# Kernel optimization log

Hardware: AMD Instinct MI355X
Metric: run time of the kernel (lower is better)

Reference implementation:

```python
import jax, jax.numpy as jnp
import numpy as np

N_USER = 100000
N_RECIPE = 50000
E = 1000000
H = 128


def setup_inputs() -> dict:
    key = jax.random.key(0)
    ks = jax.random.split(key, 5)
    z_user = jax.random.normal(ks[0], (N_USER, H), dtype=jnp.float32)
    z_recipe = jax.random.normal(ks[1], (N_RECIPE, H), dtype=jnp.float32)
    edge_label_index = jax.random.randint(ks[2], (2, E), 0, N_RECIPE, dtype=jnp.int64)
    W1 = jax.random.normal(ks[3], (2 * H, H), dtype=jnp.float32) * (1.0 / np.sqrt(2 * H))
    b1 = jnp.zeros((H,), dtype=jnp.float32)
    W2 = jax.random.normal(ks[4], (H, 1), dtype=jnp.float32) * (1.0 / np.sqrt(H))
    b2 = jnp.zeros((1,), dtype=jnp.float32)
    return {"z_user": z_user, "z_recipe": z_recipe,
            "edge_label_index": edge_label_index,
            "W1": W1, "b1": b1, "W2": W2, "b2": b2}


def reference(z_user, z_recipe, edge_label_index, W1, b1, W2, b2):
    row, col = edge_label_index[0], edge_label_index[1]
    # gather + concat: [E, 2H]
    z = jnp.concatenate([z_user[row], z_recipe[col]], axis=-1)
    h = jax.nn.relu(z @ W1 + b1)        # [E, H]
    out = h @ W2 + b2                    # [E, 1]
    return out.reshape(-1)
```

## Files before the change

kernel.cpp:

```cpp
#include <hip/hip_runtime.h>
#include <hip/hip_bf16.h>


#define HDIM 128

typedef __attribute__((ext_vector_type(8))) __bf16 bf16x8;
typedef __attribute__((ext_vector_type(16))) float f32x16;

static __device__ __forceinline__ unsigned short bf16_bits(float x) {
  return __builtin_bit_cast(unsigned short, static_cast<__bf16>(x));
}

static __device__ __forceinline__ float bf2f(unsigned short u) {
  return __builtin_bit_cast(float, ((unsigned int)u) << 16);
}

static __device__ __forceinline__ bf16x8 cvt8(float4 a, float4 b) {
  bf16x8 r;
  r[0] = static_cast<__bf16>(a.x);
  r[1] = static_cast<__bf16>(a.y);
  r[2] = static_cast<__bf16>(a.z);
  r[3] = static_cast<__bf16>(a.w);
  r[4] = static_cast<__bf16>(b.x);
  r[5] = static_cast<__bf16>(b.y);
  r[6] = static_cast<__bf16>(b.z);
  r[7] = static_cast<__bf16>(b.w);
  return r;
}

__global__ __launch_bounds__(256) void prep(const float* __restrict__ W1,
                                            unsigned short* __restrict__ W1bf,
                                            const int* __restrict__ eidx, int E,
                                            int* __restrict__ maxarr) {
  const int tid = threadIdx.x;
  const int b = blockIdx.x;
  if (b < 16 && W1bf) {
#pragma unroll
    for (int it = 0; it < 8; ++it) {
      const int idx = (b << 11) + (it << 8) + tid;
      const int k = idx >> 7;
      const int n = idx & 127;
      const int kc = k >> 4;
      const int q = (k >> 3) & 1;
      const int j = k & 7;
      const int nt = n >> 5;
      const int ln = (q << 5) | (n & 31);
      W1bf[((((kc << 2) + nt) << 6) | ln) * 8 + j] = bf16_bits(W1[idx]);
    }
  }
  int local = -1;
  for (int i = b * 256 + tid; i < E; i += 64 * 256)
    local = max(local, eidx[i]);
#pragma unroll
  for (int st = 1; st <= 32; st <<= 1)
    local = max(local, __shfl_xor(local, st));
  __shared__ int wmax[4];
  if ((tid & 63) == 0) wmax[tid >> 6] = local;
  __syncthreads();
  if (tid == 0) {
    int m = max(max(wmax[0], wmax[1]), max(wmax[2], wmax[3]));
    maxarr[b] = m;
  }
}

__global__ __launch_bounds__(256, 4) void proj_nodes(
    const float* __restrict__ zu, int NU, const float* __restrict__ zr, int NR,
    const float* __restrict__ W1, const unsigned short* __restrict__ W1bf,
    const int* __restrict__ maxarr,
    unsigned short* __restrict__ Hu, unsigned short* __restrict__ Hr,
    int ublocks) {
  __shared__ unsigned short Bsw[16384];
  const int tid = threadIdx.x;
  const bool isU = (int)blockIdx.x < ublocks;
  const int kc0 = isU ? 0 : 8;

  if (W1bf) {
    const uint4* s4 = (const uint4*)(W1bf + (kc0 << 11));
    uint4* d4 = (uint4*)Bsw;
#pragma unroll
    for (int i = 0; i < 8; ++i) d4[(i << 8) + tid] = s4[(i << 8) + tid];
  } else {
    const int n = tid & 127;
    const int kh = tid >> 7;
    const int nt = n >> 5;
    const int nl = n & 31;
#pragma unroll 8
    for (int it = 0; it < 64; ++it) {
      const int kl = 2 * it + kh;
      const float w = W1[(kc0 * 16 + kl) * HDIM + n];
      const int kc = kl >> 4;
      const int q = (kl >> 3) & 1;
      const int j = kl & 7;
      const int ln = (q << 5) | nl;
      Bsw[((((kc << 2) + nt) << 6) | ln) * 8 + j] = bf16_bits(w);
    }
  }
  __syncthreads();

  const int lane = tid & 63;
  const int wid = tid >> 6;
  const int m = lane & 31;
  const int half = lane >> 5;
  const int koff = half * 8;

  const int tl = (isU ? (int)blockIdx.x : (int)blockIdx.x - ublocks) * 4 + wid;
  const int ntype = isU ? ((NU + 31) >> 5) : ((NR + 31) >> 5);
  if (tl >= ntype) return;

  const int base = tl << 5;

  if (isU && maxarr) {
    int v = maxarr[lane];
#pragma unroll
    for (int st = 1; st <= 32; st <<= 1) v = max(v, __shfl_xor(v, st));
    if (base > v) return;
  }

  const int nmax = isU ? NU : NR;
  int node = base + m;
  if (node >= nmax) node = nmax - 1;
  const float* src = (isU ? zu : zr) + (size_t)node * HDIM + koff;

  f32x16 acc[4];
#pragma unroll
  for (int nt = 0; nt < 4; ++nt) acc[nt] = (f32x16)0.0f;

#pragma unroll
  for (int kcl = 0; kcl < 8; ++kcl) {
    const float4* sa = (const float4*)(src + kcl * 16);
    const bf16x8 a = cvt8(sa[0], sa[1]);
#pragma unroll
    for (int nt = 0; nt < 4; ++nt) {
      const uint4* bp =
          (const uint4*)(Bsw + ((((kcl << 2) + nt) << 6) | lane) * 8);
      const bf16x8 bfr = __builtin_bit_cast(bf16x8, *bp);
      acc[nt] = __builtin_amdgcn_mfma_f32_32x32x16_bf16(a, bfr, acc[nt], 0, 0, 0);
    }
  }

  unsigned short* H = isU ? Hu : Hr;
#pragma unroll
  for (int nt = 0; nt < 4; ++nt) {
#pragma unroll
    for (int r = 0; r < 16; ++r) {
      const int row = (r & 3) + ((r >> 2) << 3) + (half << 2);
      const int nrow = base + row;
      if (nrow < nmax)
        H[(size_t)nrow * HDIM + (nt << 5) + m] = bf16_bits(acc[nt][r]);
    }
  }
}

static __device__ __forceinline__ float dot8(uint4 a, uint4 b,
                                             const float* b1c,
                                             const float* w2c) {
  const unsigned short* pa = (const unsigned short*)&a;
  const unsigned short* pb = (const unsigned short*)&b;
  float s = 0.f;
#pragma unroll
  for (int j = 0; j < 8; ++j) {
    const float h = bf2f(pa[j]) + bf2f(pb[j]) + b1c[j];
    s = fmaf(fmaxf(h, 0.f), w2c[j], s);
  }
  return s;
}

__global__ __launch_bounds__(256, 4) void edge_pass(
    const unsigned short* __restrict__ Hu, const unsigned short* __restrict__ Hr,
    const int* __restrict__ eidx, const float* __restrict__ b1,
    const float* __restrict__ W2, const float* __restrict__ b2,
    float* __restrict__ out, int E) {
  const int tid = threadIdx.x;
  const int lane = tid & 63;
  const int c = lane & 15;
  const int g = lane >> 4;
  const int wid = blockIdx.x * 4 + (tid >> 6);
  const int stride = gridDim.x * 4 * 16;

  float b1c[8], w2c[8];
#pragma unroll
  for (int j = 0; j < 8; ++j) {
    b1c[j] = b1[c * 8 + j];
    w2c[j] = W2[c * 8 + j];
  }
  const float b2v = b2[0];
  const int co = c * 8;

  int e = wid * 16 + g * 4;
  if (e >= E) return;
  int iu0 = eidx[e],     ir0 = eidx[E + e];
  int iu1 = eidx[e + 1], ir1 = eidx[E + e + 1];
  int iu2 = eidx[e + 2], ir2 = eidx[E + e + 2];
  int iu3 = eidx[e + 3], ir3 = eidx[E + e + 3];

  while (true) {
    const int en = e + stride;
    const bool more = en < E;
    const int ep = more ? en : e;

    const uint4 au0 = *(const uint4*)(Hu + (size_t)iu0 * HDIM + co);
    const uint4 ar0 = *(const uint4*)(Hr + (size_t)ir0 * HDIM + co);
    const uint4 au1 = *(const uint4*)(Hu + (size_t)iu1 * HDIM + co);
    const uint4 ar1 = *(const uint4*)(Hr + (size_t)ir1 * HDIM + co);
    const uint4 au2 = *(const uint4*)(Hu + (size_t)iu2 * HDIM + co);
    const uint4 ar2 = *(const uint4*)(Hr + (size_t)ir2 * HDIM + co);
    const uint4 au3 = *(const uint4*)(Hu + (size_t)iu3 * HDIM + co);
    const uint4 ar3 = *(const uint4*)(Hr + (size_t)ir3 * HDIM + co);

    const int niu0 = eidx[ep],     nir0 = eidx[E + ep];
    const int niu1 = eidx[ep + 1], nir1 = eidx[E + ep + 1];
    const int niu2 = eidx[ep + 2], nir2 = eidx[E + ep + 2];
    const int niu3 = eidx[ep + 3], nir3 = eidx[E + ep + 3];

    float s0 = dot8(au0, ar0, b1c, w2c);
    float s1 = dot8(au1, ar1, b1c, w2c);
    float s2 = dot8(au2, ar2, b1c, w2c);
    float s3 = dot8(au3, ar3, b1c, w2c);
#pragma unroll
    for (int st = 1; st <= 8; st <<= 1) {
      s0 += __shfl_xor(s0, st);
      s1 += __shfl_xor(s1, st);
      s2 += __shfl_xor(s2, st);
      s3 += __shfl_xor(s3, st);
    }
    if (c == 0) {
      out[e]     = s0 + b2v;
      out[e + 1] = s1 + b2v;
      out[e + 2] = s2 + b2v;
      out[e + 3] = s3 + b2v;
    }
    if (!more) break;
    e = en;
    iu0 = niu0; ir0 = nir0; iu1 = niu1; ir1 = nir1;
    iu2 = niu2; ir2 = nir2; iu3 = niu3; ir3 = nir3;
  }
}

__global__ __launch_bounds__(256, 2) void edge_decoder_mfma(
    const float* __restrict__ zu, const float* __restrict__ zr,
    const int* __restrict__ eidx, const float* __restrict__ W1,
    const float* __restrict__ b1, const float* __restrict__ W2,
    const float* __restrict__ b2, float* __restrict__ out, int E) {
  __shared__ unsigned short Bsw[32768];
  const int tid = threadIdx.x;
  {
    const int n = tid & 127;
    const int kh = tid >> 7;
    const int nt = n >> 5;
    const int nl = n & 31;
#pragma unroll 8
    for (int it = 0; it < 128; ++it) {
      const int k = 2 * it + kh;
      const float w = W1[k * HDIM + n];
      const int kc = k >> 4;
      const int q = (k >> 3) & 1;
      const int j = k & 7;
      const int ln = (q << 5) | nl;
      Bsw[((((kc << 2) + nt) << 6) | ln) * 8 + j] = bf16_bits(w);
    }
  }
  __syncthreads();

  const int lane = tid & 63;
  const int wid = tid >> 6;
  const int m = lane & 31;
  const int half = lane >> 5;
  const int nsweep = E >> 6;
  const int wstride = gridDim.x * 4;

  float b1v[4], w2v[4];
#pragma unroll
  for (int nt = 0; nt < 4; ++nt) {
    b1v[nt] = b1[nt * 32 + m];
    w2v[nt] = W2[nt * 32 + m];
  }
  const float b2v = b2[0];
  const int koff = half * 8;

  for (int s = blockIdx.x * 4 + wid; s < nsweep; s += wstride) {
    const int e0 = s << 6;
    const int eA = e0 + m;
    const int eB = e0 + 32 + m;
    const float* puA = zu + (size_t)eidx[eA] * HDIM;
    const float* prA = zr + (size_t)eidx[E + eA] * HDIM;
    const float* puB = zu + (size_t)eidx[eB] * HDIM;
    const float* prB = zr + (size_t)eidx[E + eB] * HDIM;

    f32x16 acc[2][4];
#pragma unroll
    for (int mt = 0; mt < 2; ++mt)
#pragma unroll
      for (int nt = 0; nt < 4; ++nt) acc[mt][nt] = (f32x16)0.0f;

#pragma unroll
    for (int kc = 0; kc < 16; ++kc) {
      const float* srcA = (kc < 8) ? (puA + kc * 16 + koff) : (prA + (kc - 8) * 16 + koff);
      const float* srcB = (kc < 8) ? (puB + kc * 16 + koff) : (prB + (kc - 8) * 16 + koff);
      const float4* sa = (const float4*)srcA;
      const float4* sb = (const float4*)srcB;
      const bf16x8 a0 = cvt8(sa[0], sa[1]);
      const bf16x8 a1 = cvt8(sb[0], sb[1]);
#pragma unroll
      for (int nt = 0; nt < 4; ++nt) {
        const uint4* bp = (const uint4*)(Bsw + ((((kc << 2) + nt) << 6) | lane) * 8);
        const bf16x8 bfr = __builtin_bit_cast(bf16x8, *bp);
        acc[0][nt] = __builtin_amdgcn_mfma_f32_32x32x16_bf16(a0, bfr, acc[0][nt], 0, 0, 0);
        acc[1][nt] = __builtin_amdgcn_mfma_f32_32x32x16_bf16(a1, bfr, acc[1][nt], 0, 0, 0);
      }
    }

    float p0[16], p1[16];
#pragma unroll
    for (int r = 0; r < 16; ++r) { p0[r] = 0.f; p1[r] = 0.f; }
#pragma unroll
    for (int nt = 0; nt < 4; ++nt) {
#pragma unroll
      for (int r = 0; r < 16; ++r) {
        float h0 = fmaxf(acc[0][nt][r] + b1v[nt], 0.f);
        float h1 = fmaxf(acc[1][nt][r] + b1v[nt], 0.f);
        p0[r] = fmaf(h0, w2v[nt], p0[r]);
        p1[r] = fmaf(h1, w2v[nt], p1[r]);
      }
    }
#pragma unroll
    for (int st = 1; st <= 16; st <<= 1) {
#pragma unroll
      for (int r = 0; r < 16; ++r) {
        p0[r] += __shfl_xor(p0[r], st);
        p1[r] += __shfl_xor(p1[r], st);
      }
    }
    const int sel = lane & 15;
    const int mtw = (lane >> 4) & 1;
    float val = 0.f;
#pragma unroll
    for (int r = 0; r < 16; ++r) {
      const float cand = mtw ? p1[r] : p0[r];
      val = (sel == r) ? cand : val;
    }
    const int mrow = (sel & 3) + ((sel >> 2) << 3) + (half << 2);
    out[e0 + (mtw << 5) + mrow] = val + b2v;
  }
}

extern "C" void kernel_launch(void* const* d_in, const int* in_sizes, int n_in,
                              void* d_out, int out_size, void* d_ws,
                              size_t ws_size, hipStream_t stream) {
  const float* zu = (const float*)d_in[0];
  const float* zr = (const float*)d_in[1];
  const int* eidx = (const int*)d_in[2];
  const float* W1 = (const float*)d_in[3];
  const float* b1 = (const float*)d_in[4];
  const float* W2 = (const float*)d_in[5];
  const float* b2 = (const float*)d_in[6];
  float* out = (float*)d_out;
  const int nu = in_sizes[0];
  const int nr = in_sizes[1];
  const int E = in_sizes[2] / 2;
  const int NU = nu / HDIM, NR = nr / HDIM;

  const size_t needH = (size_t)(nu + nr) * sizeof(unsigned short);
  const size_t needW = 32768 * sizeof(unsigned short);
  const size_t needM = 64 * sizeof(int);

  if (ws_size >= needH) {
    unsigned short* Hu = (unsigned short*)d_ws;
    unsigned short* Hr = Hu + (size_t)nu;
    unsigned short* W1bf = nullptr;
    int* maxarr = nullptr;
    if (ws_size >= needH + needW + needM) {
      W1bf = Hr + (size_t)nr;
      maxarr = (int*)(W1bf + 32768);
      hipLaunchKernelGGL(prep, dim3(64), dim3(256), 0, stream,
                         W1, W1bf, eidx, E, maxarr);
    }
    const int utiles = (NU + 31) >> 5;
    const int rtiles = (NR + 31) >> 5;
    const int ub = (utiles + 3) >> 2;
    const int rb = (rtiles + 3) >> 2;
    hipLaunchKernelGGL(proj_nodes, dim3(ub + rb), dim3(256), 0, stream,
                       zu, NU, zr, NR, W1, W1bf, maxarr, Hu, Hr, ub);
    hipLaunchKernelGGL(edge_pass, dim3(4096), dim3(256), 0, stream,
                       Hu, Hr, eidx, b1, W2, b2, out, E);
  } else {
    hipLaunchKernelGGL(edge_decoder_mfma, dim3(512), dim3(256), 0, stream,
                       zu, zr, eidx, W1, b1, W2, b2, out, E);
  }
}
```

Measured before the change: 192.6 us.

## Fuse prep, node projection and edge pass into one cooperative persistent kernel

Replaces three separate kernel launches with a single cooperative kernel of 1024 blocks that uses grid-wide syncs between the W1 conversion and max-index scan, the node projection with MFMA, and the edge gather-dot pass. This removes launch gaps and inter-kernel tails. The cost is persistent-loop scheduling of the projection tiles across a fixed grid and two grid barriers. Unlike the old single-kernel max reduction, every block loads 32KB of LDS for Bsw even when not needed, which may limit occupancy. If the cooperative launch fails, the code falls back to the old path.

```diff
diff --git a/kernel.cpp b/kernel.cpp
--- a/kernel.cpp
+++ b/kernel.cpp
@@ -1,8 +1,12 @@
 #include <hip/hip_runtime.h>
 #include <hip/hip_bf16.h>
+#include <hip/hip_cooperative_groups.h>
+
+namespace cg = cooperative_groups;
 
 
 #define HDIM 128
+#define GRID_COOP 1024
 
 typedef __attribute__((ext_vector_type(8))) __bf16 bf16x8;
 typedef __attribute__((ext_vector_type(16))) float f32x16;
@@ -26,6 +30,197 @@
   r[6] = static_cast<__bf16>(b.z);
   r[7] = static_cast<__bf16>(b.w);
   return r;
+}
+
+static __device__ __forceinline__ float dot8(uint4 a, uint4 b,
+                                             const float* b1c,
+                                             const float* w2c) {
+  const unsigned short* pa = (const unsigned short*)&a;
+  const unsigned short* pb = (const unsigned short*)&b;
+  float s = 0.f;
+#pragma unroll
+  for (int j = 0; j < 8; ++j) {
+    const float h = bf2f(pa[j]) + bf2f(pb[j]) + b1c[j];
+    s = fmaf(fmaxf(h, 0.f), w2c[j], s);
+  }
+  return s;
+}
+
+__global__ __launch_bounds__(256, 4) void fused_all(
+    const float* __restrict__ zu, int NU, const float* __restrict__ zr, int NR,
+    const float* __restrict__ W1, unsigned short* __restrict__ W1bf,
+    int* __restrict__ maxarr, unsigned short* __restrict__ Hu,
+    unsigned short* __restrict__ Hr, const int* __restrict__ eidx, int E,
+    const float* __restrict__ b1, const float* __restrict__ W2,
+    const float* __restrict__ b2, float* __restrict__ out, int ublk) {
+  cg::grid_group grid = cg::this_grid();
+  __shared__ unsigned short Bsw[16384];
+  const int tid = threadIdx.x;
+  const int bid = blockIdx.x;
+  const int lane = tid & 63;
+  const int wid = tid >> 6;
+
+  if (bid < 16) {
+#pragma unroll
+    for (int it = 0; it < 8; ++it) {
+      const int idx = (bid << 11) + (it << 8) + tid;
+      const int k = idx >> 7;
+      const int n = idx & 127;
+      const int kc = k >> 4;
+      const int q = (k >> 3) & 1;
+      const int j = k & 7;
+      const int nt = n >> 5;
+      const int ln = (q << 5) | (n & 31);
+      W1bf[((((kc << 2) + nt) << 6) | ln) * 8 + j] = bf16_bits(W1[idx]);
+    }
+  }
+  if (bid < 64) {
+    int local = -1;
+    for (int i = bid * 256 + tid; i < E; i += 64 * 256)
+      local = max(local, eidx[i]);
+#pragma unroll
+    for (int st = 1; st <= 32; st <<= 1)
+      local = max(local, __shfl_xor(local, st));
+    __shared__ int wmax[4];
+    if ((tid & 63) == 0) wmax[tid >> 6] = local;
+    __syncthreads();
+    if (tid == 0)
+      maxarr[bid] = max(max(wmax[0], wmax[1]), max(wmax[2], wmax[3]));
+  }
+  __threadfence();
+  grid.sync();
+
+  const bool isU = bid < ublk;
+  const int kc0 = isU ? 0 : 8;
+  {
+    const uint4* s4 = (const uint4*)(W1bf + (kc0 << 11));
+    uint4* d4 = (uint4*)Bsw;
+#pragma unroll
+    for (int i = 0; i < 8; ++i) d4[(i << 8) + tid] = s4[(i << 8) + tid];
+  }
+  __syncthreads();
+
+  const int m = lane & 31;
+  const int half = lane >> 5;
+  const int koff = half * 8;
+
+  int vmax = 0x7fffffff;
+  if (isU) {
+    int v = maxarr[lane];
+#pragma unroll
+    for (int st = 1; st <= 32; st <<= 1) v = max(v, __shfl_xor(v, st));
+    vmax = v;
+  }
+
+  const int ntiles = isU ? ((NU + 31) >> 5) : ((NR + 31) >> 5);
+  const int nmax = isU ? NU : NR;
+  const float* zsrc = isU ? zu : zr;
+  unsigned short* H = isU ? Hu : Hr;
+  const int wbase = (isU ? bid : bid - ublk) * 4 + wid;
+  const int wstride = (isU ? ublk : (GRID_COOP - ublk)) * 4;
+
+  for (int t = wbase; t < ntiles; t += wstride) {
+    const int base = t << 5;
+    if (isU && base > vmax) continue;
+    int node = base + m;
+    if (node >= nmax) node = nmax - 1;
+    const float* src = zsrc + (size_t)node * HDIM + koff;
+
+    f32x16 acc[4];
+#pragma unroll
+    for (int nt = 0; nt < 4; ++nt) acc[nt] = (f32x16)0.0f;
+
+#pragma unroll
+    for (int kcl = 0; kcl < 8; ++kcl) {
+      const float4* sa = (const float4*)(src + kcl * 16);
+      const bf16x8 a = cvt8(sa[0], sa[1]);
+#pragma unroll
+      for (int nt = 0; nt < 4; ++nt) {
+        const uint4* bp =
+            (const uint4*)(Bsw + ((((kcl << 2) + nt) << 6) | lane) * 8);
+        const bf16x8 bfr = __builtin_bit_cast(bf16x8, *bp);
+        acc[nt] =
+            __builtin_amdgcn_mfma_f32_32x32x16_bf16(a, bfr, acc[nt], 0, 0, 0);
+      }
+    }
+
+#pragma unroll
+    for (int nt = 0; nt < 4; ++nt) {
+#pragma unroll
+      for (int r = 0; r < 16; ++r) {
+        const int row = (r & 3) + ((r >> 2) << 3) + (half << 2);
+        const int nrow = base + row;
+        if (nrow < nmax)
+          H[(size_t)nrow * HDIM + (nt << 5) + m] = bf16_bits(acc[nt][r]);
+      }
+    }
+  }
+  __threadfence();
+  grid.sync();
+
+  const int c = lane & 15;
+  const int g4 = lane >> 4;
+  const int ewid = bid * 4 + wid;
+  const int estride = GRID_COOP * 4 * 16;
+
+  float b1c[8], w2c[8];
+#pragma unroll
+  for (int j = 0; j < 8; ++j) {
+    b1c[j] = b1[c * 8 + j];
+    w2c[j] = W2[c * 8 + j];
+  }
+  const float b2v = b2[0];
+  const int co = c * 8;
+
+  int e = ewid * 16 + g4 * 4;
+  if (e < E) {
+    int iu0 = eidx[e],     ir0 = eidx[E + e];
+    int iu1 = eidx[e + 1], ir1 = eidx[E + e + 1];
+    int iu2 = eidx[e + 2], ir2 = eidx[E + e + 2];
+    int iu3 = eidx[e + 3], ir3 = eidx[E + e + 3];
+
+    while (true) {
+      const int en = e + estride;
+      const bool more = en < E;
+      const int ep = more ? en : e;
+
+      const uint4 au0 = *(const uint4*)(Hu + (size_t)iu0 * HDIM + co);
+      const uint4 ar0 = *(const uint4*)(Hr + (size_t)ir0 * HDIM + co);
+      const uint4 au1 = *(const uint4*)(Hu + (size_t)iu1 * HDIM + co);
+      const uint4 ar1 = *(const uint4*)(Hr + (size_t)ir1 * HDIM + co);
+      const uint4 au2 = *(const uint4*)(Hu + (size_t)iu2 * HDIM + co);
+      const uint4 ar2 = *(const uint4*)(Hr + (size_t)ir2 * HDIM + co);
+      const uint4 au3 = *(const uint4*)(Hu + (size_t)iu3 * HDIM + co);
+      const uint4 ar3 = *(const uint4*)(Hr + (size_t)ir3 * HDIM + co);
+
+      const int niu0 = eidx[ep],     nir0 = eidx[E + ep];
+      const int niu1 = eidx[ep + 1], nir1 = eidx[E + ep + 1];
+      const int niu2 = eidx[ep + 2], nir2 = eidx[E + ep + 2];
+      const int niu3 = eidx[ep + 3], nir3 = eidx[E + ep + 3];
+
+      float s0 = dot8(au0, ar0, b1c, w2c);
+      float s1 = dot8(au1, ar1, b1c, w2c);
+      float s2 = dot8(au2, ar2, b1c, w2c);
+      float s3 = dot8(au3, ar3, b1c, w2c);
+#pragma unroll
+      for (int st = 1; st <= 8; st <<= 1) {
+        s0 += __shfl_xor(s0, st);
+        s1 += __shfl_xor(s1, st);
+        s2 += __shfl_xor(s2, st);
+        s3 += __shfl_xor(s3, st);
+      }
+      if (c == 0) {
+        out[e]     = s0 + b2v;
+        out[e + 1] = s1 + b2v;
+        out[e + 2] = s2 + b2v;
+        out[e + 3] = s3 + b2v;
+      }
+      if (!more) break;
+      e = en;
+      iu0 = niu0; ir0 = nir0; iu1 = niu1; ir1 = nir1;
+      iu2 = niu2; ir2 = nir2; iu3 = niu3; ir3 = nir3;
+    }
+  }
 }
 
 __global__ __launch_bounds__(256) void prep(const float* __restrict__ W1,
@@ -108,7 +303,6 @@
   if (tl >= ntype) return;
 
   const int base = tl << 5;
-
   if (isU && maxarr) {
     int v = maxarr[lane];
 #pragma unroll
@@ -149,20 +343,6 @@
         H[(size_t)nrow * HDIM + (nt << 5) + m] = bf16_bits(acc[nt][r]);
     }
   }
-}
-
-static __device__ __forceinline__ float dot8(uint4 a, uint4 b,
-                                             const float* b1c,
-                                             const float* w2c) {
-  const unsigned short* pa = (const unsigned short*)&a;
-  const unsigned short* pb = (const unsigned short*)&b;
-  float s = 0.f;
-#pragma unroll
-  for (int j = 0; j < 8; ++j) {
-    const float h = bf2f(pa[j]) + bf2f(pb[j]) + b1c[j];
-    s = fmaf(fmaxf(h, 0.f), w2c[j], s);
-  }
-  return s;
 }
 
 __global__ __launch_bounds__(256, 4) void edge_pass(
@@ -357,11 +537,32 @@
   const int nu = in_sizes[0];
   const int nr = in_sizes[1];
   const int E = in_sizes[2] / 2;
-  const int NU = nu / HDIM, NR = nr / HDIM;
+  int NU = nu / HDIM, NR = nr / HDIM;
 
   const size_t needH = (size_t)(nu + nr) * sizeof(unsigned short);
   const size_t needW = 32768 * sizeof(unsigned short);
   const size_t needM = 64 * sizeof(int);
+
+  if (ws_size >= needH + needW + needM) {
+    unsigned short* Hu = (unsigned short*)d_ws;
+    unsigned short* Hr = Hu + (size_t)nu;
+    unsigned short* W1bf = Hr + (size_t)nr;
+    int* maxarr = (int*)(W1bf + 32768);
+    const int utiles = (NU + 31) >> 5;
+    const int rtiles = (NR + 31) >> 5;
+    int ublk = (int)((long long)GRID_COOP * utiles / (utiles + rtiles));
+    if (ublk < 1) ublk = 1;
+    if (ublk > GRID_COOP - 1) ublk = GRID_COOP - 1;
+
+    void* args[] = {(void*)&zu, (void*)&NU, (void*)&zr, (void*)&NR,
+                    (void*)&W1, (void*)&W1bf, (void*)&maxarr, (void*)&Hu,
+                    (void*)&Hr, (void*)&eidx, (void*)&E, (void*)&b1,
+                    (void*)&W2, (void*)&b2, (void*)&out, (void*)&ublk};
+    hipError_t st = hipLaunchCooperativeKernel(
+        (const void*)fused_all, dim3(GRID_COOP), dim3(256), args, 0, stream);
+    if (st == hipSuccess) return;
+    (void)hipGetLastError();
+  }
 
   if (ws_size >= needH) {
     unsigned short* Hu = (unsigned short*)d_ws;
```

Measured after the change: 619.0 us. 3.21x slower.
